# Kernel tuning notes

Hardware: AMD Instinct MI355X
Metric: run time of the kernel (lower is better)

The kernel has to match this reference:

```python
import jax, jax.numpy as jnp
import numpy as np


def setup_inputs() -> dict:
    key = jax.random.key(0)
    B, S, TYPE_RANGE = 8192, 8192, 8
    max_pred_types = jax.random.randint(key, (B, S), 0, TYPE_RANGE, dtype=jnp.int32)
    return {"max_pred_types": max_pred_types, "type_range": TYPE_RANGE}


def reference(max_pred_types, type_range):
    # max_pred_types: [B, S] int32 token ids in [0, type_range)
    B, S = max_pred_types.shape

    # rg1 / rg2: penalty if first token != 0 or second token != 1
    rg1 = jnp.sum((max_pred_types[:, 0] != 0).astype(jnp.int32) * 4)
    rg2 = jnp.sum((max_pred_types[:, 1] != 1).astype(jnp.int32) * 4)

    # rg3: (type_range - unique_count_per_row)**2, via per-row presence scatter
    rows = jnp.arange(B, dtype=jnp.int32)[:, None]              # [B,1]
    vals = jnp.clip(max_pred_types, 0, type_range - 1)          # safety clip
    present = jnp.zeros((B, type_range), dtype=jnp.int32).at[rows, vals].set(1)
    n_unique = jnp.sum(present, axis=1)                          # [B]
    rg3 = jnp.sum((type_range - n_unique) ** 2)

    # rg4: last occurrence of token 1; check 5 following tokens match [2,4,5,6,3]
    pos = jnp.arange(S, dtype=jnp.int32)[None, :]                # [1,S]
    last_1 = jnp.max(jnp.where(max_pred_types == 1, pos, -1), axis=1)  # [B], -1 if none
    cond = (last_1 > 0) & (last_1 < S - 5)
    safe = jnp.clip(last_1, 0, S - 6)
    idx = safe[:, None] + jnp.arange(1, 6, dtype=jnp.int32)[None, :]   # [B,5]
    gathered = jnp.take_along_axis(max_pred_types, idx, axis=1)        # [B,5]
    expected = jnp.array([2, 4, 5, 6, 3], dtype=max_pred_types.dtype)
    mism = jnp.sum((gathered != expected).astype(jnp.int32), axis=1)   # [B]
    rg4 = jnp.sum(jnp.where(cond, mism, 6))

    return rg1 + rg2 + rg3 + rg4
```

## Files before the change

### kernel.cpp

```cpp
#include <hip/hip_runtime.h>

__global__ __launch_bounds__(256) void row_check_kernel(
    const int* __restrict__ x, int* __restrict__ partial, int S) {
  const int row = blockIdx.x;
  const size_t rowoff = (size_t)row * (size_t)S;
  const int4* rp = (const int4*)(x + rowoff);
  const int t = threadIdx.x;

  unsigned pres = 0;
  int last1 = -1;
  int rg12 = 0;

  #pragma unroll
  for (int k = 0; k < 8; ++k) {
    const int c = t + (k << 8);
    const int4 v = rp[c];
    const int base = c << 2;
    const int e0 = v.x, e1 = v.y, e2 = v.z, e3 = v.w;
    const int c0 = min(max(e0, 0), 7), c1 = min(max(e1, 0), 7);
    const int c2 = min(max(e2, 0), 7), c3 = min(max(e3, 0), 7);
    pres |= (1u << c0) | (1u << c1) | (1u << c2) | (1u << c3);
    last1 = max(last1, (e0 == 1) ? (base + 0) : -1);
    last1 = max(last1, (e1 == 1) ? (base + 1) : -1);
    last1 = max(last1, (e2 == 1) ? (base + 2) : -1);
    last1 = max(last1, (e3 == 1) ? (base + 3) : -1);
    if (k == 0 && t == 0) {
      rg12 = ((e0 != 0) ? 4 : 0) + ((e1 != 1) ? 4 : 0);
    }
  }

  #pragma unroll
  for (int off = 32; off > 0; off >>= 1) {
    pres |= (unsigned)__shfl_down((int)pres, off);
    last1 = max(last1, __shfl_down(last1, off));
  }

  __shared__ unsigned spres[4];
  __shared__ int slast[4];
  const int wave = t >> 6;
  if ((t & 63) == 0) { spres[wave] = pres; slast[wave] = last1; }
  __syncthreads();

  if (t == 0) {
    const unsigned p = spres[0] | spres[1] | spres[2] | spres[3];
    const int l1 = max(max(slast[0], slast[1]), max(slast[2], slast[3]));
    const int d = 8 - __popc(p);
    const int rg3 = d * d;
    int rg4;
    if (l1 > 0 && l1 < S - 5) {
      const int* r = x + rowoff + l1;
      rg4 = (int)(r[1] != 2) + (int)(r[2] != 4) + (int)(r[3] != 5) +
            (int)(r[4] != 6) + (int)(r[5] != 3);
    } else {
      rg4 = 6;
    }
    partial[row] = rg12 + rg3 + rg4;
  }
}

__global__ __launch_bounds__(256) void final_reduce_kernel(
    const int* __restrict__ partial, int* __restrict__ out, int B) {
  const int t = threadIdx.x;
  int s = 0;
  for (int i = t; i < B; i += 256) s += partial[i];
  #pragma unroll
  for (int off = 32; off > 0; off >>= 1) s += __shfl_down(s, off);
  __shared__ int sw[4];
  if ((t & 63) == 0) sw[t >> 6] = s;
  __syncthreads();
  if (t == 0) out[0] = sw[0] + sw[1] + sw[2] + sw[3];
}

extern "C" void kernel_launch(void* const* d_in, const int* in_sizes, int n_in,
                              void* d_out, int out_size, void* d_ws, size_t ws_size,
                              hipStream_t stream) {
  const int* x = (const int*)d_in[0];
  const int S = 8192;
  const int B = in_sizes[0] / S;
  int* partial = (int*)d_ws;
  int* out = (int*)d_out;
  row_check_kernel<<<dim3(B), dim3(256), 0, stream>>>(x, partial, S);
  final_reduce_kernel<<<dim3(1), dim3(256), 0, stream>>>(partial, out, B);
}
```

Baseline: 357.3 us.

## Assign one row per wavefront with register double-buffered loads

Each wavefront now handles a whole row instead of a 256-thread block handling one row, which removes the shared-memory cross-wave reduction and the block barrier. Loads are software-pipelined: the next 8 int4 chunks are fetched into registers while the current 8 are processed. This raises register use and cuts the grid to a quarter as many blocks. It also hardcodes S=8192 and assumes B is divisible by 4.

```diff
diff --git a/kernel.cpp b/kernel.cpp
--- a/kernel.cpp
+++ b/kernel.cpp
@@ -1,31 +1,47 @@
 #include <hip/hip_runtime.h>
 
 __global__ __launch_bounds__(256) void row_check_kernel(
-    const int* __restrict__ x, int* __restrict__ partial, int S) {
-  const int row = blockIdx.x;
-  const size_t rowoff = (size_t)row * (size_t)S;
+    const int* __restrict__ x, int* __restrict__ partial) {
+  const int wave = threadIdx.x >> 6;
+  const int lane = threadIdx.x & 63;
+  const int row  = (blockIdx.x << 2) + wave;
+  const size_t rowoff = (size_t)row << 13;
   const int4* rp = (const int4*)(x + rowoff);
-  const int t = threadIdx.x;
 
   unsigned pres = 0;
   int last1 = -1;
   int rg12 = 0;
 
+  int4 buf[8];
   #pragma unroll
-  for (int k = 0; k < 8; ++k) {
-    const int c = t + (k << 8);
-    const int4 v = rp[c];
-    const int base = c << 2;
-    const int e0 = v.x, e1 = v.y, e2 = v.z, e3 = v.w;
-    const int c0 = min(max(e0, 0), 7), c1 = min(max(e1, 0), 7);
-    const int c2 = min(max(e2, 0), 7), c3 = min(max(e3, 0), 7);
-    pres |= (1u << c0) | (1u << c1) | (1u << c2) | (1u << c3);
-    last1 = max(last1, (e0 == 1) ? (base + 0) : -1);
-    last1 = max(last1, (e1 == 1) ? (base + 1) : -1);
-    last1 = max(last1, (e2 == 1) ? (base + 2) : -1);
-    last1 = max(last1, (e3 == 1) ? (base + 3) : -1);
-    if (k == 0 && t == 0) {
-      rg12 = ((e0 != 0) ? 4 : 0) + ((e1 != 1) ? 4 : 0);
+  for (int j = 0; j < 8; ++j) buf[j] = rp[lane + (j << 6)];
+
+  #pragma unroll
+  for (int g = 0; g < 4; ++g) {
+    int4 nxt[8];
+    if (g < 3) {
+      #pragma unroll
+      for (int j = 0; j < 8; ++j) nxt[j] = rp[lane + (((g + 1) * 8 + j) << 6)];
+    }
+    #pragma unroll
+    for (int j = 0; j < 8; ++j) {
+      const int4 v = buf[j];
+      const int base = (lane + ((g * 8 + j) << 6)) << 2;
+      const int e0 = v.x, e1 = v.y, e2 = v.z, e3 = v.w;
+      const int c0 = min(max(e0, 0), 7), c1 = min(max(e1, 0), 7);
+      const int c2 = min(max(e2, 0), 7), c3 = min(max(e3, 0), 7);
+      pres |= (1u << c0) | (1u << c1) | (1u << c2) | (1u << c3);
+      last1 = max(last1, (e0 == 1) ? (base + 0) : -1);
+      last1 = max(last1, (e1 == 1) ? (base + 1) : -1);
+      last1 = max(last1, (e2 == 1) ? (base + 2) : -1);
+      last1 = max(last1, (e3 == 1) ? (base + 3) : -1);
+      if (g == 0 && j == 0 && lane == 0) {
+        rg12 = ((e0 != 0) ? 4 : 0) + ((e1 != 1) ? 4 : 0);
+      }
+    }
+    if (g < 3) {
+      #pragma unroll
+      for (int j = 0; j < 8; ++j) buf[j] = nxt[j];
     }
   }
 
@@ -35,24 +51,14 @@
     last1 = max(last1, __shfl_down(last1, off));
   }
 
-  __shared__ unsigned spres[4];
-  __shared__ int slast[4];
-  const int wave = t >> 6;
-  if ((t & 63) == 0) { spres[wave] = pres; slast[wave] = last1; }
-  __syncthreads();
-
-  if (t == 0) {
-    const unsigned p = spres[0] | spres[1] | spres[2] | spres[3];
-    const int l1 = max(max(slast[0], slast[1]), max(slast[2], slast[3]));
-    const int d = 8 - __popc(p);
+  if (lane == 0) {
+    const int d = 8 - __popc(pres);
     const int rg3 = d * d;
-    int rg4;
-    if (l1 > 0 && l1 < S - 5) {
-      const int* r = x + rowoff + l1;
+    int rg4 = 6;
+    if (last1 > 0 && last1 < 8192 - 5) {
+      const int* r = x + rowoff + last1;
       rg4 = (int)(r[1] != 2) + (int)(r[2] != 4) + (int)(r[3] != 5) +
             (int)(r[4] != 6) + (int)(r[5] != 3);
-    } else {
-      rg4 = 6;
     }
     partial[row] = rg12 + rg3 + rg4;
   }
@@ -79,6 +85,6 @@
   const int B = in_sizes[0] / S;
   int* partial = (int*)d_ws;
   int* out = (int*)d_out;
-  row_check_kernel<<<dim3(B), dim3(256), 0, stream>>>(x, partial, S);
+  row_check_kernel<<<dim3(B / 4), dim3(256), 0, stream>>>(x, partial);
   final_reduce_kernel<<<dim3(1), dim3(256), 0, stream>>>(partial, out, B);
 }
```

After: 354.5 us (median of 2 runs). About the same (-0.8%).
